# Performance work log

Measured on AMD Instinct MI355X. Metric: run time of the kernel, lower is better.

## Reference

```python
import jax, jax.numpy as jnp
import numpy as np

N_NODES = 50000
N_EDGES = 800000
IN_FEAT = 512
OUT_FEAT = 128


def multispike(x):
    return jnp.floor(jnp.clip(4.0 * x, 0.0, 4.0) + 0.5) / 4.0


def setup_inputs() -> dict:
    key = jax.random.key(0)
    k1, k2, k3, k4, k5 = jax.random.split(key, 5)
    feat = jax.random.normal(k1, (N_NODES, IN_FEAT), dtype=jnp.float32)
    # Xavier-uniform-like init for the weight parameter
    limit = np.sqrt(6.0 / (IN_FEAT + OUT_FEAT)).astype(np.float32)
    weight = jax.random.uniform(k2, (IN_FEAT, OUT_FEAT), dtype=jnp.float32,
                                minval=-limit, maxval=limit)
    rows = jnp.sort(jax.random.randint(k3, (N_EDGES,), 0, N_NODES, dtype=jnp.int32))
    cols = jax.random.randint(k4, (N_EDGES,), 0, N_NODES, dtype=jnp.int32)
    edge_weight = jax.random.uniform(k5, (N_EDGES,), dtype=jnp.float32)
    return {"feat": feat, "weight": weight, "rows": rows, "cols": cols,
            "edge_weight": edge_weight}


def reference(feat, weight, rows, cols, edge_weight):
    # x = feat @ W                     [N, out_feat]
    x = jnp.matmul(feat, weight)
    # x = spmm(adj, x): out[i] = sum_{e: rows[e]==i} w_e * x[cols[e]]
    edge_feats = edge_weight[:, None] * x[cols]          # [E, out_feat]
    x = jax.ops.segment_sum(edge_feats, rows, num_segments=N_NODES)
    # quantized multi-spike activation
    return multispike(x)
```

## Files before the change

kernel.cpp:

```cpp
#include <hip/hip_runtime.h>

#define N_NODES 50000
#define N_EDGES 800000
#define IN_FEAT 512
#define OUT_FEAT 128

__device__ __forceinline__ float multispike(float a) {
    return floorf(fminf(fmaxf(4.0f * a, 0.0f), 4.0f) + 0.5f) * 0.25f;
}

__global__ __launch_bounds__(256) void gemm_kernel(const float* __restrict__ A,
                                                   const float* __restrict__ B,
                                                   float* __restrict__ C, int M) {
    __shared__ float As[32][64];
    __shared__ float Bs[32][128];

    const int tid = threadIdx.x;
    const int tx = tid & 31;
    const int ty = tid >> 5;
    const int block_m = blockIdx.x * 64;

    float acc[8][4];
#pragma unroll
    for (int i = 0; i < 8; i++)
#pragma unroll
        for (int j = 0; j < 4; j++) acc[i][j] = 0.0f;

    for (int k0 = 0; k0 < IN_FEAT; k0 += 32) {
#pragma unroll
        for (int i = 0; i < 2; i++) {
            int f = tid + i * 256;
            int r = f >> 3;
            int kq = (f & 7) << 2;
            int gm = block_m + r;
            float4 v = make_float4(0.f, 0.f, 0.f, 0.f);
            if (gm < M) v = *(const float4*)(A + (size_t)gm * IN_FEAT + k0 + kq);
            As[kq + 0][r] = v.x;
            As[kq + 1][r] = v.y;
            As[kq + 2][r] = v.z;
            As[kq + 3][r] = v.w;
        }
#pragma unroll
        for (int i = 0; i < 4; i++) {
            int f = tid + i * 256;
            int r = f >> 5;
            int n4 = (f & 31) << 2;
            *(float4*)&Bs[r][n4] = *(const float4*)(B + (size_t)(k0 + r) * OUT_FEAT + n4);
        }
        __syncthreads();

#pragma unroll
        for (int k = 0; k < 32; k++) {
            float4 a0 = *(const float4*)&As[k][ty * 8];
            float4 a1 = *(const float4*)&As[k][ty * 8 + 4];
            float4 b = *(const float4*)&Bs[k][tx * 4];
            float av[8] = {a0.x, a0.y, a0.z, a0.w, a1.x, a1.y, a1.z, a1.w};
            float bv[4] = {b.x, b.y, b.z, b.w};
#pragma unroll
            for (int i = 0; i < 8; i++)
#pragma unroll
                for (int j = 0; j < 4; j++)
                    acc[i][j] = fmaf(av[i], bv[j], acc[i][j]);
        }
        __syncthreads();
    }

#pragma unroll
    for (int i = 0; i < 8; i++) {
        int gm = block_m + ty * 8 + i;
        if (gm < M) {
            float4 v = make_float4(acc[i][0], acc[i][1], acc[i][2], acc[i][3]);
            *(float4*)(C + (size_t)gm * OUT_FEAT + tx * 4) = v;
        }
    }
}

__global__ __launch_bounds__(256) void rowptr_kernel(const int* __restrict__ rows,
                                                     int* __restrict__ row_ptr) {
    int i = blockIdx.x * blockDim.x + threadIdx.x;
    if (i > N_NODES) return;
    int lo = 0, hi = N_EDGES;
    while (lo < hi) {
        int mid = (lo + hi) >> 1;
        if (rows[mid] < i) lo = mid + 1; else hi = mid;
    }
    row_ptr[i] = lo;
}

__global__ __launch_bounds__(256) void spmm_kernel(const float* __restrict__ x,
                                                   const int* __restrict__ cols,
                                                   const float* __restrict__ ew,
                                                   const int* __restrict__ row_ptr,
                                                   float* __restrict__ out) {
    const int wave = threadIdx.x >> 6;
    const int lane = threadIdx.x & 63;
    const int r = blockIdx.x * 4 + wave;
    if (r >= N_NODES) return;

    const int e0 = row_ptr[r];
    const int e1 = row_ptr[r + 1];

    float acc0 = 0.0f, acc1 = 0.0f;
    for (int e = e0; e < e1; e++) {
        int c = cols[e];
        float w = ew[e];
        const float* xp = x + (size_t)c * OUT_FEAT;
        acc0 = fmaf(w, xp[lane], acc0);
        acc1 = fmaf(w, xp[lane + 64], acc1);
    }
    out[(size_t)r * OUT_FEAT + lane] = multispike(acc0);
    out[(size_t)r * OUT_FEAT + lane + 64] = multispike(acc1);
}

extern "C" void kernel_launch(void* const* d_in, const int* in_sizes, int n_in,
                              void* d_out, int out_size, void* d_ws, size_t ws_size,
                              hipStream_t stream) {
    const float* feat = (const float*)d_in[0];
    const float* weight = (const float*)d_in[1];
    const int* rows = (const int*)d_in[2];
    const int* cols = (const int*)d_in[3];
    const float* ew = (const float*)d_in[4];
    float* out = (float*)d_out;

    float* x = (float*)d_ws;
    int* row_ptr = (int*)((char*)d_ws + (size_t)N_NODES * OUT_FEAT * sizeof(float));

    rowptr_kernel<<<(N_NODES + 256) / 256, 256, 0, stream>>>(rows, row_ptr);
    gemm_kernel<<<(N_NODES + 63) / 64, 256, 0, stream>>>(feat, weight, x, N_NODES);
    spmm_kernel<<<(N_NODES + 3) / 4, 256, 0, stream>>>(x, cols, ew, row_ptr, out);
}
```

Baseline: 326.5 us.

## Prefetch GEMM tiles into registers, pad shared A, vectorize and unroll SpMM gather

The GEMM now loads the next K-tile from global memory into registers while computing on the current shared-memory tile, which hides global load latency. The transposed A tile gets padding to reduce LDS bank conflicts on its scattered stores. The SpMM gathers each neighbour row as float2 per lane and unrolls the edge loop by four, so several independent gathers are in flight at once. The cost is more registers in both kernels, and the accumulation order in SpMM changes slightly.

```diff
diff --git a/kernel.cpp b/kernel.cpp
--- a/kernel.cpp
+++ b/kernel.cpp
@@ -12,7 +12,7 @@
 __global__ __launch_bounds__(256) void gemm_kernel(const float* __restrict__ A,
                                                    const float* __restrict__ B,
                                                    float* __restrict__ C, int M) {
-    __shared__ float As[32][64];
+    __shared__ float As[32][68];
     __shared__ float Bs[32][128];
 
     const int tid = threadIdx.x;
@@ -20,34 +20,64 @@
     const int ty = tid >> 5;
     const int block_m = blockIdx.x * 64;
 
+    const int a_r0 = tid >> 3;
+    const int a_kq = (tid & 7) << 2;
+    const int b_n4 = (tid & 31) << 2;
+    const int b_r0 = tid >> 5;
+
     float acc[8][4];
 #pragma unroll
     for (int i = 0; i < 8; i++)
 #pragma unroll
         for (int j = 0; j < 4; j++) acc[i][j] = 0.0f;
 
-    for (int k0 = 0; k0 < IN_FEAT; k0 += 32) {
+    float4 pa[2];
+    float4 pb[4];
+
+    {
+        const int k0 = 0;
 #pragma unroll
         for (int i = 0; i < 2; i++) {
-            int f = tid + i * 256;
-            int r = f >> 3;
-            int kq = (f & 7) << 2;
-            int gm = block_m + r;
-            float4 v = make_float4(0.f, 0.f, 0.f, 0.f);
-            if (gm < M) v = *(const float4*)(A + (size_t)gm * IN_FEAT + k0 + kq);
-            As[kq + 0][r] = v.x;
-            As[kq + 1][r] = v.y;
-            As[kq + 2][r] = v.z;
-            As[kq + 3][r] = v.w;
+            int gm = block_m + a_r0 + i * 32;
+            pa[i] = make_float4(0.f, 0.f, 0.f, 0.f);
+            if (gm < M) pa[i] = *(const float4*)(A + (size_t)gm * IN_FEAT + k0 + a_kq);
         }
 #pragma unroll
         for (int i = 0; i < 4; i++) {
-            int f = tid + i * 256;
-            int r = f >> 5;
-            int n4 = (f & 31) << 2;
-            *(float4*)&Bs[r][n4] = *(const float4*)(B + (size_t)(k0 + r) * OUT_FEAT + n4);
+            int r = b_r0 + i * 8;
+            pb[i] = *(const float4*)(B + (size_t)(k0 + r) * OUT_FEAT + b_n4);
+        }
+    }
+
+    for (int t = 0; t < IN_FEAT / 32; t++) {
+#pragma unroll
+        for (int i = 0; i < 2; i++) {
+            int r = a_r0 + i * 32;
+            As[a_kq + 0][r] = pa[i].x;
+            As[a_kq + 1][r] = pa[i].y;
+            As[a_kq + 2][r] = pa[i].z;
+            As[a_kq + 3][r] = pa[i].w;
+        }
+#pragma unroll
+        for (int i = 0; i < 4; i++) {
+            *(float4*)&Bs[b_r0 + i * 8][b_n4] = pb[i];
         }
         __syncthreads();
+
+        if (t + 1 < IN_FEAT / 32) {
+            const int k0 = (t + 1) * 32;
+#pragma unroll
+            for (int i = 0; i < 2; i++) {
+                int gm = block_m + a_r0 + i * 32;
+                pa[i] = make_float4(0.f, 0.f, 0.f, 0.f);
+                if (gm < M) pa[i] = *(const float4*)(A + (size_t)gm * IN_FEAT + k0 + a_kq);
+            }
+#pragma unroll
+            for (int i = 0; i < 4; i++) {
+                int r = b_r0 + i * 8;
+                pb[i] = *(const float4*)(B + (size_t)(k0 + r) * OUT_FEAT + b_n4);
+            }
+        }
 
 #pragma unroll
         for (int k = 0; k < 32; k++) {
@@ -99,17 +129,31 @@
 
     const int e0 = row_ptr[r];
     const int e1 = row_ptr[r + 1];
+    const float2* __restrict__ x2 = (const float2*)x;
 
-    float acc0 = 0.0f, acc1 = 0.0f;
-    for (int e = e0; e < e1; e++) {
+    float accx = 0.0f, accy = 0.0f;
+    int e = e0;
+    for (; e + 4 <= e1; e += 4) {
+        int c0 = cols[e], c1 = cols[e + 1], c2 = cols[e + 2], c3 = cols[e + 3];
+        float w0 = ew[e], w1 = ew[e + 1], w2 = ew[e + 2], w3 = ew[e + 3];
+        float2 v0 = x2[(size_t)c0 * 64 + lane];
+        float2 v1 = x2[(size_t)c1 * 64 + lane];
+        float2 v2 = x2[(size_t)c2 * 64 + lane];
+        float2 v3 = x2[(size_t)c3 * 64 + lane];
+        accx = fmaf(w0, v0.x, accx); accy = fmaf(w0, v0.y, accy);
+        accx = fmaf(w1, v1.x, accx); accy = fmaf(w1, v1.y, accy);
+        accx = fmaf(w2, v2.x, accx); accy = fmaf(w2, v2.y, accy);
+        accx = fmaf(w3, v3.x, accx); accy = fmaf(w3, v3.y, accy);
+    }
+    for (; e < e1; e++) {
         int c = cols[e];
         float w = ew[e];
-        const float* xp = x + (size_t)c * OUT_FEAT;
-        acc0 = fmaf(w, xp[lane], acc0);
-        acc1 = fmaf(w, xp[lane + 64], acc1);
+        float2 v = x2[(size_t)c * 64 + lane];
+        accx = fmaf(w, v.x, accx);
+        accy = fmaf(w, v.y, accy);
     }
-    out[(size_t)r * OUT_FEAT + lane] = multispike(acc0);
-    out[(size_t)r * OUT_FEAT + lane + 64] = multispike(acc1);
+    float2* out2 = (float2*)out;
+    out2[(size_t)r * 64 + lane] = make_float2(multispike(accx), multispike(accy));
 }
 
 extern "C" void kernel_launch(void* const* d_in, const int* in_sizes, int n_in,
```

New measurement: 317.5 us. 2.8% less time.

## Enlarge GEMM register tile with swizzled B smem and unroll SpMM gathers

Applied to the files above, without the earlier changes.

The GEMM now uses 128 threads per block, each computing an 8x8 output tile instead of 8x4. B is stored in shared memory with an XOR swizzle and A is padded to cut bank conflicts, which raises FMA work per shared-memory load. The SpMM batches eight edges at a time, loading indices and weights first and then issuing the float2 gathers together, so more memory requests are in flight. The trade-off is more registers per thread and fewer threads per GEMM block, which may lower occupancy.

```diff
diff --git a/kernel.cpp b/kernel.cpp
--- a/kernel.cpp
+++ b/kernel.cpp
@@ -5,31 +5,37 @@
 #define IN_FEAT 512
 #define OUT_FEAT 128
 
+
 __device__ __forceinline__ float multispike(float a) {
     return floorf(fminf(fmaxf(4.0f * a, 0.0f), 4.0f) + 0.5f) * 0.25f;
 }
 
-__global__ __launch_bounds__(256) void gemm_kernel(const float* __restrict__ A,
+__device__ __forceinline__ int bswz(int q) { return q ^ ((q >> 3) & 1); }
+
+__global__ __launch_bounds__(128) void gemm_kernel(const float* __restrict__ A,
                                                    const float* __restrict__ B,
                                                    float* __restrict__ C, int M) {
-    __shared__ float As[32][64];
+    __shared__ float As[32][68];
     __shared__ float Bs[32][128];
 
     const int tid = threadIdx.x;
-    const int tx = tid & 31;
-    const int ty = tid >> 5;
+    const int tx = tid & 15;
+    const int ty = tid >> 4;
     const int block_m = blockIdx.x * 64;
 
-    float acc[8][4];
+    const int bq0 = bswz(2 * tx) * 4;
+    const int bq1 = bswz(2 * tx + 1) * 4;
+
+    float acc[8][8];
 #pragma unroll
     for (int i = 0; i < 8; i++)
 #pragma unroll
-        for (int j = 0; j < 4; j++) acc[i][j] = 0.0f;
+        for (int j = 0; j < 8; j++) acc[i][j] = 0.0f;
 
     for (int k0 = 0; k0 < IN_FEAT; k0 += 32) {
 #pragma unroll
-        for (int i = 0; i < 2; i++) {
-            int f = tid + i * 256;
+        for (int i = 0; i < 4; i++) {
+            int f = tid + i * 128;
             int r = f >> 3;
             int kq = (f & 7) << 2;
             int gm = block_m + r;
@@ -41,11 +47,12 @@
             As[kq + 3][r] = v.w;
         }
 #pragma unroll
-        for (int i = 0; i < 4; i++) {
-            int f = tid + i * 256;
+        for (int i = 0; i < 8; i++) {
+            int f = tid + i * 128;
             int r = f >> 5;
-            int n4 = (f & 31) << 2;
-            *(float4*)&Bs[r][n4] = *(const float4*)(B + (size_t)(k0 + r) * OUT_FEAT + n4);
+            int q = f & 31;
+            *(float4*)&Bs[r][bswz(q) * 4] =
+                *(const float4*)(B + (size_t)(k0 + r) * OUT_FEAT + q * 4);
         }
         __syncthreads();
 
@@ -53,13 +60,14 @@
         for (int k = 0; k < 32; k++) {
             float4 a0 = *(const float4*)&As[k][ty * 8];
             float4 a1 = *(const float4*)&As[k][ty * 8 + 4];
-            float4 b = *(const float4*)&Bs[k][tx * 4];
+            float4 b0 = *(const float4*)&Bs[k][bq0];
+            float4 b1 = *(const float4*)&Bs[k][bq1];
             float av[8] = {a0.x, a0.y, a0.z, a0.w, a1.x, a1.y, a1.z, a1.w};
-            float bv[4] = {b.x, b.y, b.z, b.w};
+            float bv[8] = {b0.x, b0.y, b0.z, b0.w, b1.x, b1.y, b1.z, b1.w};
 #pragma unroll
             for (int i = 0; i < 8; i++)
 #pragma unroll
-                for (int j = 0; j < 4; j++)
+                for (int j = 0; j < 8; j++)
                     acc[i][j] = fmaf(av[i], bv[j], acc[i][j]);
         }
         __syncthreads();
@@ -69,8 +77,9 @@
     for (int i = 0; i < 8; i++) {
         int gm = block_m + ty * 8 + i;
         if (gm < M) {
-            float4 v = make_float4(acc[i][0], acc[i][1], acc[i][2], acc[i][3]);
-            *(float4*)(C + (size_t)gm * OUT_FEAT + tx * 4) = v;
+            float* cp = C + (size_t)gm * OUT_FEAT + tx * 8;
+            *(float4*)cp = make_float4(acc[i][0], acc[i][1], acc[i][2], acc[i][3]);
+            *(float4*)(cp + 4) = make_float4(acc[i][4], acc[i][5], acc[i][6], acc[i][7]);
         }
     }
 }
@@ -99,17 +108,38 @@
 
     const int e0 = row_ptr[r];
     const int e1 = row_ptr[r + 1];
+    const float2* __restrict__ x2 = (const float2*)x;
 
-    float acc0 = 0.0f, acc1 = 0.0f;
-    for (int e = e0; e < e1; e++) {
+    float accx = 0.0f, accy = 0.0f;
+    int e = e0;
+    for (; e + 8 <= e1; e += 8) {
+        int c[8];
+        float w[8];
+        float2 v[8];
+#pragma unroll
+        for (int j = 0; j < 8; j++) {
+            c[j] = cols[e + j];
+            w[j] = ew[e + j];
+        }
+#pragma unroll
+        for (int j = 0; j < 8; j++) {
+            v[j] = x2[(size_t)c[j] * 64 + lane];
+        }
+#pragma unroll
+        for (int j = 0; j < 8; j++) {
+            accx = fmaf(w[j], v[j].x, accx);
+            accy = fmaf(w[j], v[j].y, accy);
+        }
+    }
+    for (; e < e1; e++) {
         int c = cols[e];
         float w = ew[e];
-        const float* xp = x + (size_t)c * OUT_FEAT;
-        acc0 = fmaf(w, xp[lane], acc0);
-        acc1 = fmaf(w, xp[lane + 64], acc1);
+        float2 v = x2[(size_t)c * 64 + lane];
+        accx = fmaf(w, v.x, accx);
+        accy = fmaf(w, v.y, accy);
     }
-    out[(size_t)r * OUT_FEAT + lane] = multispike(acc0);
-    out[(size_t)r * OUT_FEAT + lane + 64] = multispike(acc1);
+    float2* out2 = (float2*)out;
+    out2[(size_t)r * 64 + lane] = make_float2(multispike(accx), multispike(accy));
 }
 
 extern "C" void kernel_launch(void* const* d_in, const int* in_sizes, int n_in,
@@ -126,6 +156,6 @@
     int* row_ptr = (int*)((char*)d_ws + (size_t)N_NODES * OUT_FEAT * sizeof(float));
 
     rowptr_kernel<<<(N_NODES + 256) / 256, 256, 0, stream>>>(rows, row_ptr);
-    gemm_kernel<<<(N_NODES + 63) / 64, 256, 0, stream>>>(feat, weight, x, N_NODES);
+    gemm_kernel<<<(N_NODES + 63) / 64, 128, 0, stream>>>(feat, weight, x, N_NODES);
     spmm_kernel<<<(N_NODES + 3) / 4, 256, 0, stream>>>(x, cols, ew, row_ptr, out);
 }
```

Result: faster. 316.2 us (-3.1%).
